# Kernel tuning notes

Hardware: AMD Instinct MI355X
Metric: run time of the kernel (lower is better)

## Reference

```python
import jax, jax.numpy as jnp
import numpy as np

B, S, HID = 2, 2048, 2048
H, KV, D = 16, 4, 128
ROT = 64           # partial rotary dim (= cos.shape[-1])
EMB = 128          # router embedding dim
TAU, BASE = 0.4, 3.0
EPS = 1e-6


def rotate_half(x):
    h = x.shape[-1] // 2
    return jnp.concatenate([-x[..., h:], x[..., :h]], axis=-1)


def rmsnorm(x, w, eps=EPS):
    # Qwen3.5: zero-init weight, (1 + w) scaling, compute in fp32
    xf = x.astype(jnp.float32)
    o = xf * jax.lax.rsqrt(jnp.mean(xf * xf, axis=-1, keepdims=True) + eps)
    return (o * (1.0 + w.astype(jnp.float32))).astype(x.dtype)


def _rope_tables():
    inv_freq = 1.0 / (10000.0 ** (np.arange(0, ROT, 2, dtype=np.float32) / ROT))
    t = np.arange(S, dtype=np.float32)
    freqs = np.outer(t, inv_freq)                 # [S, ROT/2]
    emb = np.concatenate([freqs, freqs], axis=-1)  # [S, ROT]
    cos = np.broadcast_to(np.cos(emb), (B, S, ROT)).copy()
    sin = np.broadcast_to(np.sin(emb), (B, S, ROT)).copy()
    return jnp.asarray(cos), jnp.asarray(sin)


def setup_inputs() -> dict:
    key = jax.random.key(0)
    ks = jax.random.split(key, 10)
    sc = 0.02
    cos, sin = _rope_tables()
    return {
        "hidden_states": jax.random.normal(ks[0], (B, S, HID), jnp.float32),
        "cos": cos,
        "sin": sin,
        # projection weights stored as [in, out] (torch Linear weight transposed)
        "Wq": jax.random.normal(ks[1], (HID, H * D * 2), jnp.float32) * sc,
        "Wk": jax.random.normal(ks[2], (HID, KV * D), jnp.float32) * sc,
        "Wv": jax.random.normal(ks[3], (HID, KV * D), jnp.float32) * sc,
        "Wo": jax.random.normal(ks[4], (H * D, HID), jnp.float32) * sc,
        "q_norm_w": jnp.zeros((D,), jnp.float32),
        "k_norm_w": jnp.zeros((D,), jnp.float32),
        "Wr": jax.random.normal(ks[5], (HID, EMB), jnp.float32) * sc,   # router linear
        "Wd": jax.random.normal(ks[6], (EMB, D), jnp.float32) * sc,     # router decoder
        "ln_g": jnp.ones((EMB,), jnp.float32),
        "ln_b": jnp.zeros((EMB,), jnp.float32),
        "rnn_state": jnp.zeros((EMB,), jnp.float32),
    }


def _forward(hidden_states, cos, sin, Wq, Wk, Wv, Wo, q_norm_w, k_norm_w,
             Wr, Wd, ln_g, ln_b, rnn_state):
    b, s, _ = hidden_states.shape
    # doubled q_proj -> query + gate
    qkv = jnp.einsum('bsh,hd->bsd', hidden_states, Wq).reshape(b, s, H, 2 * D)
    q, gate = qkv[..., :D], qkv[..., D:]
    gate = gate.reshape(b, s, H * D)
    k = jnp.einsum('bsh,hd->bsd', hidden_states, Wk).reshape(b, s, KV, D)
    v = jnp.einsum('bsh,hd->bsd', hidden_states, Wv).reshape(b, s, KV, D)
    # per-head RMSNorm then [b, h, s, d]
    q = rmsnorm(q, q_norm_w).transpose(0, 2, 1, 3)
    k = rmsnorm(k, k_norm_w).transpose(0, 2, 1, 3)
    v = v.transpose(0, 2, 1, 3)

    # --- head-dim router (gumbel-sigmoid, straight-through hard round) ---
    emb = jnp.einsum('bsh,he->bse', hidden_states, Wr) + rnn_state
    mu = jnp.mean(emb, -1, keepdims=True)
    var = jnp.mean((emb - mu) ** 2, -1, keepdims=True)
    ln = (emb - mu) * jax.lax.rsqrt(var + 1e-5) * ln_g + ln_b
    logits = jnp.einsum('bse,ed->bsd', jax.nn.gelu(ln, approximate=False), Wd)
    gum = -jnp.log(jax.random.exponential(jax.random.key(42), logits.shape, jnp.float32))
    y_soft = jax.nn.sigmoid((logits + gum + BASE) / TAU)
    binary = jax.lax.stop_gradient(jnp.round(y_soft) - y_soft) + y_soft  # [b, s, D]
    mask = binary[:, None, :, :]  # broadcast over heads: [b, 1, s, D]

    q = q * mask
    k = k * mask

    # partial RoPE on first ROT dims (qk_index=None training path)
    c = cos[:, None, :, :]
    si = sin[:, None, :, :]
    def rope(x):
        xr, xp = x[..., :ROT], x[..., ROT:]
        return jnp.concatenate([xr * c + rotate_half(xr) * si, xp], axis=-1)
    q = rope(q)
    k = rope(k)

    # GQA: repeat kv heads
    rep = H // KV
    k = jnp.repeat(k, rep, axis=1)
    v = jnp.repeat(v, rep, axis=1)

    scores = jnp.einsum('bhqd,bhkd->bhqk', q, k) / np.sqrt(D).astype(np.float32)
    causal = jnp.tril(jnp.ones((s, s), bool))
    scores = jnp.where(causal, scores, jnp.finfo(jnp.float32).min)
    attn = jax.nn.softmax(scores.astype(jnp.float32), axis=-1).astype(q.dtype)
    out = jnp.einsum('bhqk,bhkd->bhqd', attn, v)
    out = out.transpose(0, 2, 1, 3).reshape(b, s, H * D)
    out = out * jax.nn.sigmoid(gate)   # output gate
    return jnp.einsum('bsd,dh->bsh', out, Wo)


def reference(hidden_states, cos, sin, Wq, Wk, Wv, Wo, q_norm_w, k_norm_w,
              Wr, Wd, ln_g, ln_b, rnn_state):
    return _forward(hidden_states, cos, sin, Wq, Wk, Wv, Wo, q_norm_w, k_norm_w,
                    Wr, Wd, ln_g, ln_b, rnn_state)
```

## Files before the change

### kernel.cpp

```cpp
#include <hip/hip_runtime.h>
#include <math.h>

typedef __bf16 bf16;
typedef bf16 bf16x8 __attribute__((ext_vector_type(8)));
typedef bf16 bf16x4 __attribute__((ext_vector_type(4)));
typedef float f32x4 __attribute__((ext_vector_type(4)));

#define BB 2
#define SS 2048
#define HIDN 2048
#define NH 16
#define NKV 4
#define DD 128
#define NROT 64
#define NPROJ 5248

__device__ __forceinline__ float waveAllReduceSum(float v) {
#pragma unroll
  for (int o = 1; o < 64; o <<= 1) v += __shfl_xor(v, o, 64);
  return v;
}

__device__ __forceinline__ int xcd_swz(int orig, int nwg) {
  return (orig & 7) * (nwg >> 3) + (orig >> 3);
}

__device__ __forceinline__ void gload16(const bf16* g, bf16* l) {
  __builtin_amdgcn_global_load_lds((const __attribute__((address_space(1))) void*)g,
                                   (__attribute__((address_space(3))) void*)l, 16, 0, 0);
}

__device__ __forceinline__ void do_transpose(bf16 (*tile)[72], const float* __restrict__ W,
                                             bf16* __restrict__ WT, int K, int N, int rowOff,
                                             int bx, int by, int t) {
  int n0 = bx * 64, k0 = by * 64;
  int tx = t & 63, ty = t >> 6;
#pragma unroll
  for (int i = 0; i < 16; i++) {
    int k = ty + i * 4;
    tile[k][tx] = (bf16)W[(size_t)(k0 + k) * N + n0 + tx];
  }
  __syncthreads();
#pragma unroll
  for (int i = 0; i < 16; i++) {
    int n = ty + i * 4;
    WT[(size_t)(rowOff + n0 + n) * K + k0 + tx] = tile[tx][n];
  }
}

__global__ __launch_bounds__(256) void prep_weights(const float* __restrict__ hidden,
                                                    const float* __restrict__ Wq,
                                                    const float* __restrict__ Wk,
                                                    const float* __restrict__ Wv,
                                                    const float* __restrict__ Wr,
                                                    const float* __restrict__ Wo,
                                                    bf16* __restrict__ hb,
                                                    bf16* __restrict__ WTall,
                                                    bf16* __restrict__ WoT) {
  __shared__ bf16 tile[64][72];
  int id = blockIdx.x, t = threadIdx.x;
  if (id < 4096) {
    int i = (id * 256 + t) * 8;
    float4 v0 = *reinterpret_cast<const float4*>(hidden + i);
    float4 v1 = *reinterpret_cast<const float4*>(hidden + i + 4);
    bf16x8 o = {(bf16)v0.x, (bf16)v0.y, (bf16)v0.z, (bf16)v0.w,
                (bf16)v1.x, (bf16)v1.y, (bf16)v1.z, (bf16)v1.w};
    *reinterpret_cast<bf16x8*>(hb + i) = o;
    return;
  }
  int id2 = id - 4096;
  if (id2 < 2048) { do_transpose(tile, Wq, WTall, 2048, 4096, 0, id2 & 63, id2 >> 6, t); return; }
  id2 -= 2048;
  if (id2 < 256) { do_transpose(tile, Wk, WTall, 2048, 512, 4096, id2 & 7, id2 >> 3, t); return; }
  id2 -= 256;
  if (id2 < 256) { do_transpose(tile, Wv, WTall, 2048, 512, 4608, id2 & 7, id2 >> 3, t); return; }
  id2 -= 256;
  if (id2 < 64) { do_transpose(tile, Wr, WTall, 2048, 128, 5120, id2 & 1, id2 >> 1, t); return; }
  id2 -= 64;
  do_transpose(tile, Wo, WoT, 2048, 2048, 0, id2 & 31, id2 >> 5, t);
}

template <typename CT>
__global__ __launch_bounds__(256) void gemm_bt(const bf16* __restrict__ A,
                                               const bf16* __restrict__ Bt,
                                               CT* __restrict__ C, int M, int N, int K) {
  __shared__ bf16 lA[128 * 64];
  __shared__ bf16 lB[128 * 64];
  const int nbx = N >> 7;
  int wg = xcd_swz(blockIdx.x, gridDim.x);
  int bx = wg % nbx, by = wg / nbx;
  const int t = threadIdx.x;
  const int l = t & 63, w = t >> 6;
  const int wr = w >> 1, wc = w & 1;
  const int lr = l & 15, lhi = l >> 4;

  f32x4 acc[4][4];
#pragma unroll
  for (int m = 0; m < 4; m++)
#pragma unroll
    for (int n = 0; n < 4; n++) acc[m][n] = f32x4{0.f, 0.f, 0.f, 0.f};

  const int rowA0 = by * 128, rowB0 = bx * 128;
  const int nkt = K >> 6;
  for (int kt = 0; kt < nkt; ++kt) {
    __syncthreads();
#pragma unroll
    for (int it = 0; it < 4; ++it) {
      int slot = it * 256 + t;
      int row = slot >> 3, sl = slot & 7;
      gload16(A + (size_t)(rowA0 + row) * K + kt * 64 + ((sl ^ (row & 7)) << 3), lA + slot * 8);
      gload16(Bt + (size_t)(rowB0 + row) * K + kt * 64 + ((sl ^ (row & 7)) << 3), lB + slot * 8);
    }
    __syncthreads();
#pragma unroll
    for (int kc = 0; kc < 2; ++kc) {
      bf16x8 af[4], bg[4];
#pragma unroll
      for (int m = 0; m < 4; m++) {
        int row = wr * 64 + m * 16 + lr;
        af[m] = *reinterpret_cast<const bf16x8*>((char*)lA + row * 128 + (((kc * 4 + lhi) ^ (row & 7)) << 4));
      }
#pragma unroll
      for (int n = 0; n < 4; n++) {
        int row = wc * 64 + n * 16 + lr;
        bg[n] = *reinterpret_cast<const bf16x8*>((char*)lB + row * 128 + (((kc * 4 + lhi) ^ (row & 7)) << 4));
      }
      __builtin_amdgcn_s_setprio(1);
#pragma unroll
      for (int m = 0; m < 4; m++)
#pragma unroll
        for (int n = 0; n < 4; n++)
          acc[m][n] = __builtin_amdgcn_mfma_f32_16x16x32_bf16(af[m], bg[n], acc[m][n], 0, 0, 0);
      __builtin_amdgcn_s_setprio(0);
    }
  }
#pragma unroll
  for (int m = 0; m < 4; m++)
#pragma unroll
    for (int n = 0; n < 4; n++)
#pragma unroll
      for (int r = 0; r < 4; r++) {
        int grow = rowA0 + wr * 64 + m * 16 + lhi * 4 + r;
        int gcol = rowB0 + wc * 64 + n * 16 + lr;
        C[(size_t)grow * N + gcol] = (CT)acc[m][n][r];
      }
}

__device__ __forceinline__ unsigned rotl32(unsigned x, int r) { return (x << r) | (x >> (32 - r)); }

__device__ __forceinline__ float gumbel42(unsigned i) {
  const unsigned half = (unsigned)(BB * SS * DD) / 2u;
  unsigned x0, x1;
  int word;
  if (i < half) { x0 = i; x1 = i + half; word = 0; }
  else          { x0 = i - half; x1 = i; word = 1; }
  const unsigned k0 = 0u, k1 = 42u;
  const unsigned k2 = k0 ^ k1 ^ 0x1BD11BDAu;
  x0 += k0; x1 += k1;
#define TF_R(r) { x0 += x1; x1 = rotl32(x1, r); x1 ^= x0; }
  TF_R(13) TF_R(15) TF_R(26) TF_R(6)
  x0 += k1; x1 += k2 + 1u;
  TF_R(17) TF_R(29) TF_R(16) TF_R(24)
  x0 += k2; x1 += k0 + 2u;
  TF_R(13) TF_R(15) TF_R(26) TF_R(6)
  x0 += k0; x1 += k1 + 3u;
  TF_R(17) TF_R(29) TF_R(16) TF_R(24)
  x0 += k1; x1 += k2 + 4u;
  TF_R(13) TF_R(15) TF_R(26) TF_R(6)
  x0 += k2; x1 += k0 + 5u;
#undef TF_R
  unsigned bits = word ? x1 : x0;
  float u = __uint_as_float((bits >> 9) | 0x3f800000u) - 1.0f;
  float ex = -log1pf(-u);
  return -logf(ex);
}

__global__ __launch_bounds__(128) void mask_kernel(const bf16* __restrict__ qkva,
                                                   const float* __restrict__ rnn,
                                                   const float* __restrict__ lng,
                                                   const float* __restrict__ lnb,
                                                   const float* __restrict__ Wd,
                                                   bf16* __restrict__ maskb) {
  int row = blockIdx.x;
  int t = threadIdx.x;
  int l = t & 63, w = t >> 6;
  __shared__ float redm[2], redv[2], gsh[128];
  float e = (float)qkva[(size_t)row * NPROJ + 5120 + t] + rnn[t];
  float s1 = waveAllReduceSum(e);
  if (l == 0) redm[w] = s1;
  __syncthreads();
  float mu = (redm[0] + redm[1]) * (1.0f / 128.0f);
  float dv = (e - mu) * (e - mu);
  float s2 = waveAllReduceSum(dv);
  if (l == 0) redv[w] = s2;
  __syncthreads();
  float var = (redv[0] + redv[1]) * (1.0f / 128.0f);
  float ln = (e - mu) * rsqrtf(var + 1e-5f) * lng[t] + lnb[t];
  float g = 0.5f * ln * (1.0f + erff(ln * 0.7071067811865475f));
  gsh[t] = g;
  __syncthreads();
  float logit = 0.f;
#pragma unroll 8
  for (int e2 = 0; e2 < 128; e2++) logit += gsh[e2] * Wd[e2 * 128 + t];
  float gum = gumbel42((unsigned)(row * 128 + t));
  float x = (logit + gum + 3.0f) * 2.5f;
  float y = 1.0f / (1.0f + expf(-x));
  maskb[(size_t)row * 128 + t] = (bf16)rintf(y);
}

#define QSCALE (0.08838834764831845f * 1.4426950408889634f)

__global__ __launch_bounds__(256) void qkv_prep(const bf16* __restrict__ qkva,
                                                const bf16* __restrict__ maskb,
                                                const float* __restrict__ qw,
                                                const float* __restrict__ kw,
                                                const float* __restrict__ cosT,
                                                const float* __restrict__ sinT,
                                                bf16* __restrict__ wq,
                                                bf16* __restrict__ sgate,
                                                bf16* __restrict__ wk,
                                                bf16* __restrict__ wvt) {
  int id = blockIdx.x, t = threadIdx.x;
  if (id < 4096) {
    int g = t >> 4, ln = t & 15;
    int hr = id * 16 + g;
    int h = hr & 15, row = hr >> 4;
    int b = row >> 11, s = row & 2047;
    const bf16* qp = qkva + (size_t)row * NPROJ + h * 256 + ln * 8;
    bf16x8 q8 = *reinterpret_cast<const bf16x8*>(qp);
    bf16x8 g8 = *reinterpret_cast<const bf16x8*>(qp + 128);
    bf16x8 m8 = *reinterpret_cast<const bf16x8*>(maskb + (size_t)row * 128 + ln * 8);
    float qf[8], ss = 0.f;
#pragma unroll
    for (int j = 0; j < 8; j++) { qf[j] = (float)q8[j]; ss += qf[j] * qf[j]; }
#pragma unroll
    for (int o = 1; o < 16; o <<= 1) ss += __shfl_xor(ss, o, 16);
    float rinv = rsqrtf(ss * (1.0f / 128.0f) + 1e-6f);
    alignas(16) float wv[8];
    const float4* qw4 = reinterpret_cast<const float4*>(qw);
    *reinterpret_cast<float4*>(&wv[0]) = qw4[ln * 2];
    *reinterpret_cast<float4*>(&wv[4]) = qw4[ln * 2 + 1];
    float qm[8];
#pragma unroll
    for (int j = 0; j < 8; j++) qm[j] = qf[j] * rinv * (1.0f + wv[j]) * (float)m8[j];
    alignas(16) float c8[8], s8[8];
    if (ln < 8) {
      const float4* c4 = reinterpret_cast<const float4*>(cosT + (size_t)row * 64);
      const float4* sn4 = reinterpret_cast<const float4*>(sinT + (size_t)row * 64);
      *reinterpret_cast<float4*>(&c8[0]) = c4[ln * 2];
      *reinterpret_cast<float4*>(&c8[4]) = c4[ln * 2 + 1];
      *reinterpret_cast<float4*>(&s8[0]) = sn4[ln * 2];
      *reinterpret_cast<float4*>(&s8[4]) = sn4[ln * 2 + 1];
    }
    float po[8];
#pragma unroll
    for (int j = 0; j < 8; j++) po[j] = __shfl_xor(qm[j], 4, 16);
    bf16x8 oq, og;
#pragma unroll
    for (int j = 0; j < 8; j++) {
      float ov;
      if (ln < 4) ov = qm[j] * c8[j] - po[j] * s8[j];
      else if (ln < 8) ov = qm[j] * c8[j] + po[j] * s8[j];
      else ov = qm[j];
      oq[j] = (bf16)(ov * QSCALE);
      og[j] = (bf16)(1.0f / (1.0f + expf(-(float)g8[j])));
    }
    size_t o = ((size_t)((b * 16 + h) * 2048 + s)) * 128 + ln * 8;
    *reinterpret_cast<bf16x8*>(wq + o) = oq;
    *reinterpret_cast<bf16x8*>(sgate + o) = og;
    return;
  }
  if (id < 5120) {
    int g = t >> 4, ln = t & 15;
    int hr = (id - 4096) * 16 + g;
    int kv = hr & 3, row = hr >> 2;
    int b = row >> 11, s = row & 2047;
    const bf16* kp = qkva + (size_t)row * NPROJ + 4096 + kv * 128 + ln * 8;
    bf16x8 k8 = *reinterpret_cast<const bf16x8*>(kp);
    bf16x8 m8 = *reinterpret_cast<const bf16x8*>(maskb + (size_t)row * 128 + ln * 8);
    float kf[8], ss = 0.f;
#pragma unroll
    for (int j = 0; j < 8; j++) { kf[j] = (float)k8[j]; ss += kf[j] * kf[j]; }
#pragma unroll
    for (int o = 1; o < 16; o <<= 1) ss += __shfl_xor(ss, o, 16);
    float rinv = rsqrtf(ss * (1.0f / 128.0f) + 1e-6f);
    alignas(16) float wv[8];
    const float4* kw4 = reinterpret_cast<const float4*>(kw);
    *reinterpret_cast<float4*>(&wv[0]) = kw4[ln * 2];
    *reinterpret_cast<float4*>(&wv[4]) = kw4[ln * 2 + 1];
    float km[8];
#pragma unroll
    for (int j = 0; j < 8; j++) km[j] = kf[j] * rinv * (1.0f + wv[j]) * (float)m8[j];
    alignas(16) float c8[8], s8[8];
    if (ln < 8) {
      const float4* c4 = reinterpret_cast<const float4*>(cosT + (size_t)row * 64);
      const float4* sn4 = reinterpret_cast<const float4*>(sinT + (size_t)row * 64);
      *reinterpret_cast<float4*>(&c8[0]) = c4[ln * 2];
      *reinterpret_cast<float4*>(&c8[4]) = c4[ln * 2 + 1];
      *reinterpret_cast<float4*>(&s8[0]) = sn4[ln * 2];
      *reinterpret_cast<float4*>(&s8[4]) = sn4[ln * 2 + 1];
    }
    float po[8];
#pragma unroll
    for (int j = 0; j < 8; j++) po[j] = __shfl_xor(km[j], 4, 16);
    bf16x8 ok;
#pragma unroll
    for (int j = 0; j < 8; j++) {
      float ov;
      if (ln < 4) ov = km[j] * c8[j] - po[j] * s8[j];
      else if (ln < 8) ov = km[j] * c8[j] + po[j] * s8[j];
      else ov = km[j];
      ok[j] = (bf16)ov;
    }
    *reinterpret_cast<bf16x8*>(wk + ((size_t)((b * 4 + kv) * 2048 + s)) * 128 + ln * 8) = ok;
    return;
  }
  {
    __shared__ bf16 tl[64][72];
    int vb = id - 5120;
    int dt = vb & 1;
    int st = (vb >> 1) & 31;
    int bkv = vb >> 6;
    int b = bkv >> 2, kv = bkv & 3;
    int tx = t & 63, ty = t >> 6;
    int s0 = st * 64, d0 = dt * 64;
#pragma unroll
    for (int i = 0; i < 16; i++) {
      int srow = ty + i * 4;
      tl[srow][tx] = qkva[(size_t)(b * 2048 + s0 + srow) * NPROJ + 4608 + kv * 128 + d0 + tx];
    }
    __syncthreads();
#pragma unroll
    for (int i = 0; i < 16; i++) {
      int drow = ty + i * 4;
      wvt[(size_t)((b * 4 + kv) * 128 + d0 + drow) * 2048 + s0 + tx] = tl[tx][drow];
    }
  }
}

__global__ __launch_bounds__(512) void attn_kernel(const bf16* __restrict__ wq,
                                                   const bf16* __restrict__ wk,
                                                   const bf16* __restrict__ wvt,
                                                   const bf16* __restrict__ sgate,
                                                   bf16* __restrict__ wattn) {
  __shared__ bf16 lK[2][64 * 128];
  __shared__ bf16 lV[2][128 * 64];
  __shared__ bf16 lP[8][16 * 64];
  int wg = xcd_swz(blockIdx.x, 256);
  int pp = wg & 7;
  int bh = wg >> 3;
  int b = bh >> 4, h = bh & 15, kvh = h >> 2;
  int t = threadIdx.x, l = t & 63, w = t >> 6;
  int lr = l & 15, lhi = l >> 4;

  const bf16* kbase = wk + (size_t)((b * 4 + kvh) * 2048) * 128;
  const bf16* vbase = wvt + (size_t)((b * 4 + kvh) * 128) * 2048;
  char* pb = (char*)(&lP[w][0]);

  const int n0 = 2 * pp + 2;

  auto stage = [&](int buf, int tt) {
#pragma unroll
    for (int it = 0; it < 2; ++it) {
      int slot = it * 512 + t;
      int row = slot >> 4, sl = slot & 15;
      gload16(kbase + (size_t)(tt * 64 + row) * 128 + ((sl ^ (row & 7)) << 3), lK[buf] + slot * 8);
      int row2 = slot >> 3, sl2 = slot & 7;
      gload16(vbase + (size_t)row2 * 2048 + tt * 64 + ((sl2 ^ (row2 & 7)) << 3), lV[buf] + slot * 8);
    }
  };

  bf16x8 aq[4];
  f32x4 oacc[8];
  float m_run, l_run;
  int qb128 = pp;

  auto load_q = [&](int qbv) {
    const bf16* qbase = wq + (size_t)(bh * 2048 + qbv * 128 + w * 16) * 128;
#pragma unroll
    for (int kc = 0; kc < 4; kc++)
      aq[kc] = *reinterpret_cast<const bf16x8*>(qbase + (size_t)lr * 128 + kc * 32 + lhi * 8);
  };
  load_q(pp);
#pragma unroll
  for (int db = 0; db < 8; db++) oacc[db] = f32x4{0.f, 0.f, 0.f, 0.f};
  m_run = -3.0e38f;
  l_run = 0.f;

  stage(0, 0);
  __syncthreads();
  int cur = 0;

  for (int i = 0; i < 34; ++i) {
    int tt = (i < n0) ? i : i - n0;
    if (i + 1 < 34) {
      int tn = (i + 1 < n0) ? (i + 1) : (i + 1 - n0);
      stage(cur ^ 1, tn);
    }
    int qrow0 = qb128 * 128 + w * 16;

    f32x4 sacc[4];
#pragma unroll
    for (int j = 0; j < 4; j++) sacc[j] = f32x4{0.f, 0.f, 0.f, 0.f};
    __builtin_amdgcn_s_setprio(1);
#pragma unroll
    for (int kc = 0; kc < 4; kc++)
#pragma unroll
      for (int j = 0; j < 4; j++) {
        int row = j * 16 + lr;
        bf16x8 ak = *reinterpret_cast<const bf16x8*>((char*)lK[cur] + row * 256 + (((kc * 4 + lhi) ^ (row & 7)) << 4));
        sacc[j] = __builtin_amdgcn_mfma_f32_16x16x32_bf16(ak, aq[kc], sacc[j], 0, 0, 0);
      }
    __builtin_amdgcn_s_setprio(0);

    if (tt * 64 + 63 > qrow0) {
      int qrow_g = qrow0 + lr;
#pragma unroll
      for (int j = 0; j < 4; j++)
#pragma unroll
        for (int r = 0; r < 4; r++) {
          int kg = tt * 64 + j * 16 + lhi * 4 + r;
          if (kg > qrow_g) sacc[j][r] = -1e30f;
        }
    }

    float m0 = fmaxf(fmaxf(sacc[0][0], sacc[0][1]), fmaxf(sacc[0][2], sacc[0][3]));
    float m1 = fmaxf(fmaxf(sacc[1][0], sacc[1][1]), fmaxf(sacc[1][2], sacc[1][3]));
    float m2 = fmaxf(fmaxf(sacc[2][0], sacc[2][1]), fmaxf(sacc[2][2], sacc[2][3]));
    float m3 = fmaxf(fmaxf(sacc[3][0], sacc[3][1]), fmaxf(sacc[3][2], sacc[3][3]));
    float mx = fmaxf(fmaxf(m0, m1), fmaxf(m2, m3));
    mx = fmaxf(mx, __shfl_xor(mx, 16, 64));
    mx = fmaxf(mx, __shfl_xor(mx, 32, 64));

    if (!__all(mx <= m_run + 8.0f)) {
      float mnew = fmaxf(m_run, mx);
      float corr = exp2f(m_run - mnew);
      l_run *= corr;
      m_run = mnew;
      float corr_o[4];
#pragma unroll
      for (int r = 0; r < 4; r++) corr_o[r] = __shfl(corr, lhi * 4 + r, 64);
#pragma unroll
      for (int db = 0; db < 8; db++)
#pragma unroll
        for (int r = 0; r < 4; r++) oacc[db][r] *= corr_o[r];
    }

    float p[4][4];
    float rs = 0.f;
#pragma unroll
    for (int j = 0; j < 4; j++) {
      float s0 = 0.f;
#pragma unroll
      for (int r = 0; r < 4; r++) {
        float pv = exp2f(sacc[j][r] - m_run);
        p[j][r] = pv;
        s0 += pv;
      }
      rs += s0;
    }
    rs += __shfl_xor(rs, 16, 64);
    rs += __shfl_xor(rs, 32, 64);
    l_run += rs;

#pragma unroll
    for (int j = 0; j < 4; j++) {
      bf16x4 p4 = {(bf16)p[j][0], (bf16)p[j][1], (bf16)p[j][2], (bf16)p[j][3]};
      *reinterpret_cast<bf16x4*>(pb + lr * 128 + ((j * 32 + lhi * 8) ^ ((lr & 7) << 4))) = p4;
    }
    bf16x8 pa[2];
#pragma unroll
    for (int kc2 = 0; kc2 < 2; kc2++)
      pa[kc2] = *reinterpret_cast<const bf16x8*>(pb + lr * 128 + ((kc2 * 64 + lhi * 16) ^ ((lr & 7) << 4)));
    __builtin_amdgcn_s_setprio(1);
#pragma unroll
    for (int kc2 = 0; kc2 < 2; kc2++)
#pragma unroll
      for (int db = 0; db < 8; db++) {
        int row = db * 16 + lr;
        bf16x8 bv = *reinterpret_cast<const bf16x8*>((char*)lV[cur] + row * 128 + (((kc2 * 4 + lhi) ^ (row & 7)) << 4));
        oacc[db] = __builtin_amdgcn_mfma_f32_16x16x32_bf16(pa[kc2], bv, oacc[db], 0, 0, 0);
      }
    __builtin_amdgcn_s_setprio(0);

    if (i == n0 - 1 || i == 33) {
      float linv[4];
#pragma unroll
      for (int r = 0; r < 4; r++) linv[r] = 1.0f / __shfl(l_run, lhi * 4 + r, 64);
#pragma unroll
      for (int r = 0; r < 4; r++) {
        int srow = qb128 * 128 + w * 16 + lhi * 4 + r;
#pragma unroll
        for (int db = 0; db < 8; db++) {
          int dcol = db * 16 + lr;
          float g = (float)sgate[(size_t)(bh * 2048 + srow) * 128 + dcol];
          float ov = oacc[db][r] * linv[r] * g;
          wattn[(size_t)(b * 2048 + srow) * 2048 + h * 128 + dcol] = (bf16)ov;
        }
      }
      if (i == n0 - 1) {
        qb128 = 15 - pp;
        load_q(qb128);
#pragma unroll
        for (int db = 0; db < 8; db++) oacc[db] = f32x4{0.f, 0.f, 0.f, 0.f};
        m_run = -3.0e38f;
        l_run = 0.f;
      }
    }

    __syncthreads();
    cur ^= 1;
  }
}

extern "C" void kernel_launch(void* const* d_in, const int* in_sizes, int n_in,
                              void* d_out, int out_size, void* d_ws, size_t ws_size,
                              hipStream_t stream) {
  const float* hidden = (const float*)d_in[0];
  const float* cosT = (const float*)d_in[1];
  const float* sinT = (const float*)d_in[2];
  const float* Wq = (const float*)d_in[3];
  const float* Wk = (const float*)d_in[4];
  const float* Wv = (const float*)d_in[5];
  const float* Wo = (const float*)d_in[6];
  const float* qw = (const float*)d_in[7];
  const float* kw = (const float*)d_in[8];
  const float* Wr = (const float*)d_in[9];
  const float* Wd = (const float*)d_in[10];
  const float* lng = (const float*)d_in[11];
  const float* lnb = (const float*)d_in[12];
  const float* rnn = (const float*)d_in[13];
  float* out = (float*)d_out;

  char* p = (char*)d_ws;
  auto alloc = [&](size_t bytes) { char* r = p; p += (bytes + 255) & ~(size_t)255; return r; };
  bf16* hb    = (bf16*)alloc((size_t)4096 * 2048 * 2);
  bf16* WTall = (bf16*)alloc((size_t)NPROJ * 2048 * 2);
  bf16* WoT   = (bf16*)alloc((size_t)2048 * 2048 * 2);
  bf16* qkva  = (bf16*)alloc((size_t)4096 * NPROJ * 2);
  bf16* maskb = (bf16*)alloc((size_t)4096 * 128 * 2);
  bf16* wqb   = (bf16*)alloc((size_t)2 * 16 * 2048 * 128 * 2);
  bf16* wkb   = (bf16*)alloc((size_t)2 * 4 * 2048 * 128 * 2);
  bf16* wvtb  = (bf16*)alloc((size_t)2 * 4 * 128 * 2048 * 2);
  bf16* sgb   = (bf16*)alloc((size_t)2 * 16 * 2048 * 128 * 2);
  bf16* wab   = (bf16*)alloc((size_t)4096 * 2048 * 2);
  if ((size_t)(p - (char*)d_ws) > ws_size) return;

  prep_weights<<<7744, 256, 0, stream>>>(hidden, Wq, Wk, Wv, Wr, Wo, hb, WTall, WoT);

  gemm_bt<bf16><<<41 * 32, 256, 0, stream>>>(hb, WTall, qkva, 4096, NPROJ, 2048);

  mask_kernel<<<4096, 128, 0, stream>>>(qkva, rnn, lng, lnb, Wd, maskb);
  qkv_prep<<<5632, 256, 0, stream>>>(qkva, maskb, qw, kw, cosT, sinT, wqb, sgb, wkb, wvtb);

  attn_kernel<<<256, 512, 0, stream>>>(wqb, wkb, wvtb, sgb, wab);

  gemm_bt<float><<<16 * 32, 256, 0, stream>>>(wab, WoT, out, 4096, 2048, 2048);
}
```

Baseline: 279.2 us.

## Vectorize weight transpose and map attention blocks so each XCD shares one KV head

The weight transpose in prep_weights now loads float4 from global memory and writes 16-byte bf16x8 stores instead of scalar accesses, and adds a trailing barrier so the shared tile can be reused safely. The attention kernel drops the generic XCD swizzle and uses a custom block-to-(batch, kv head, head, part) mapping. Assuming blocks are dispatched round-robin over the 8 XCDs, all blocks that share a batch/KV-head pair land on the same XCD and reuse its L2 for K/V tiles. The column-wise LDS reads in the transpose may cause bank conflicts.

```diff
diff --git a/kernel.cpp b/kernel.cpp
--- a/kernel.cpp
+++ b/kernel.cpp
@@ -34,18 +34,29 @@
                                              bf16* __restrict__ WT, int K, int N, int rowOff,
                                              int bx, int by, int t) {
   int n0 = bx * 64, k0 = by * 64;
-  int tx = t & 63, ty = t >> 6;
-#pragma unroll
-  for (int i = 0; i < 16; i++) {
-    int k = ty + i * 4;
-    tile[k][tx] = (bf16)W[(size_t)(k0 + k) * N + n0 + tx];
+  {
+    int c4 = (t & 15) * 4, r = t >> 4;
+#pragma unroll
+    for (int p = 0; p < 4; p++) {
+      int row = p * 16 + r;
+      float4 v = *reinterpret_cast<const float4*>(W + (size_t)(k0 + row) * N + n0 + c4);
+      bf16x4 o = {(bf16)v.x, (bf16)v.y, (bf16)v.z, (bf16)v.w};
+      *reinterpret_cast<bf16x4*>(&tile[row][c4]) = o;
+    }
   }
   __syncthreads();
-#pragma unroll
-  for (int i = 0; i < 16; i++) {
-    int n = ty + i * 4;
-    WT[(size_t)(rowOff + n0 + n) * K + k0 + tx] = tile[tx][n];
-  }
+  {
+    int ln = t & 7, n = t >> 3;
+#pragma unroll
+    for (int p = 0; p < 2; p++) {
+      int nn = p * 32 + n;
+      bf16x8 o;
+#pragma unroll
+      for (int j = 0; j < 8; j++) o[j] = tile[ln * 8 + j][nn];
+      *reinterpret_cast<bf16x8*>(WT + (size_t)(rowOff + n0 + nn) * K + k0 + ln * 8) = o;
+    }
+  }
+  __syncthreads();
 }
 
 __global__ __launch_bounds__(256) void prep_weights(const float* __restrict__ hidden,
@@ -346,10 +357,13 @@
   __shared__ bf16 lK[2][64 * 128];
   __shared__ bf16 lV[2][128 * 64];
   __shared__ bf16 lP[8][16 * 64];
-  int wg = xcd_swz(blockIdx.x, 256);
-  int pp = wg & 7;
-  int bh = wg >> 3;
-  int b = bh >> 4, h = bh & 15, kvh = h >> 2;
+  int bid = blockIdx.x;
+  int grp = bid & 7;
+  int b = grp >> 2, kvh = grp & 3;
+  int g32 = bid >> 3;
+  int pp = g32 & 7;
+  int h = kvh * 4 + (g32 >> 3);
+  int bh = b * 16 + h;
   int t = threadIdx.x, l = t & 63, w = t >> 6;
   int lr = l & 15, lhi = l >> 4;
 
```

New measurement: 279.1 us. No clear change (-0.0%).
